# Kernel tuning notes

Hardware: AMD Instinct MI355X
Metric: run time of the kernel (lower is better)

Reference implementation:

```python
import jax, jax.numpy as jnp
import numpy as np

N_NODES = 100_000
N_EDGES = 3_200_000
IN_CH, HID, EMB = 8, 64, 32


def setup_inputs() -> dict:
    key = jax.random.key(0)
    ks = jax.random.split(key, 12)
    x = jax.random.normal(ks[0], (N_NODES, IN_CH), dtype=jnp.float32)
    edge_index = jax.random.randint(ks[1], (2, N_EDGES), 0, N_NODES, dtype=jnp.int64)
    s = 0.1
    return {
        "x": x,
        "edge_index": edge_index,
        # SAGEConv1: lin_l (neighbors, with bias), lin_r (root, no bias)
        "W1l": jax.random.normal(ks[2], (IN_CH, HID), jnp.float32) * s,
        "b1": jnp.zeros((HID,), jnp.float32),
        "W1r": jax.random.normal(ks[3], (IN_CH, HID), jnp.float32) * s,
        # SAGEConv2
        "W2l": jax.random.normal(ks[4], (HID, EMB), jnp.float32) * s,
        "b2": jnp.zeros((EMB,), jnp.float32),
        "W2r": jax.random.normal(ks[5], (HID, EMB), jnp.float32) * s,
        # head: Linear(32,16) ReLU Linear(16,1) Sigmoid
        "Wh1": jax.random.normal(ks[6], (EMB, 16), jnp.float32) * s,
        "bh1": jnp.zeros((16,), jnp.float32),
        "Wh2": jax.random.normal(ks[7], (16, 1), jnp.float32) * s,
        "bh2": jnp.zeros((1,), jnp.float32),
    }


def _sage_conv(x, src, dst, Wl, bl, Wr):
    # mean-aggregate source features at destination nodes
    msgs = x[src]                                            # [E, F]
    summed = jax.ops.segment_sum(msgs, dst, num_segments=N_NODES)
    cnt = jax.ops.segment_sum(jnp.ones((src.shape[0], 1), x.dtype), dst,
                              num_segments=N_NODES)
    aggr = summed / jnp.maximum(cnt, 1.0)                    # [N, F]
    return aggr @ Wl + bl + x @ Wr


def reference(x, edge_index, W1l, b1, W1r, W2l, b2, W2r, Wh1, bh1, Wh2, bh2):
    src, dst = edge_index[0], edge_index[1]
    h = jax.nn.relu(_sage_conv(x, src, dst, W1l, b1, W1r))   # [N, 64]
    z = jax.nn.relu(_sage_conv(h, src, dst, W2l, b2, W2r))   # [N, 32]
    logits = jax.nn.relu(z @ Wh1 + bh1) @ Wh2 + bh2          # [N, 1]
    return jax.nn.sigmoid(logits)[:, 0]                      # [N]
```

## Files before the change

kernel.cpp:

```cpp
#include <hip/hip_runtime.h>
#include <hip/hip_fp16.h>
#include <math.h>

#define IN_CH 8
#define HID   64
#define EMB   32
#define HBLK  256
#define BW    512
#define BSH   9
#define NBMAX 256
#define P8SCALE 128.0f
#define X8SCALE 16.0f

typedef _Float16 half2n __attribute__((ext_vector_type(2)));

static __device__ __forceinline__ __half2 u2h2(unsigned u) {
    union { unsigned u; __half2 h; } c; c.u = u; return c.h;
}
static __device__ __forceinline__ unsigned h22u(__half2 h) {
    union { unsigned u; __half2 h; } c; c.h = h; return c.u;
}
static __device__ __forceinline__ half2n u2n(unsigned u) {
    union { unsigned u; half2n h; } c; c.u = u; return c.h;
}
static __device__ __forceinline__ half2n mkh2(float a, float b) {
    half2n r; r.x = (_Float16)a; r.y = (_Float16)b; return r;
}
static __device__ __forceinline__ float fdot2w(half2n a, half2n b, float c) {
#if __has_builtin(__builtin_amdgcn_fdot2)
    return __builtin_amdgcn_fdot2(a, b, c, false);
#else
    return (float)a.x * (float)b.x + (float)a.y * (float)b.y + c;
#endif
}

__global__ __launch_bounds__(256) void histprep_kernel(
        const int* __restrict__ ei, int* __restrict__ gcnt, int* __restrict__ blkoff,
        int E, int NB, int per,
        const float* __restrict__ x, unsigned* __restrict__ x8,
        const float* __restrict__ W1l, const float* __restrict__ W1r,
        const float* __restrict__ W2l, const float* __restrict__ W2r,
        unsigned* __restrict__ w1p, unsigned* __restrict__ w2lp,
        unsigned* __restrict__ w2rp, int N) {
    __shared__ int lh[NBMAX];
    int b = blockIdx.x, t = threadIdx.x;
    if (b < HBLK) {
        for (int i = t; i < NB; i += 256) lh[i] = 0;
        __syncthreads();
        int e0 = b * per, e1 = min(e0 + per, E);
        if (e0 < e1) {
            if ((E & 3) == 0) {
                int nv = (e1 - e0) >> 2;
                for (int g = t; g < nv; g += 256) {
                    int4 d = *(const int4*)(ei + E + e0 + g * 4);
                    atomicAdd(&lh[d.x >> BSH], 1);
                    atomicAdd(&lh[d.y >> BSH], 1);
                    atomicAdd(&lh[d.z >> BSH], 1);
                    atomicAdd(&lh[d.w >> BSH], 1);
                }
                for (int e = e0 + nv * 4 + t; e < e1; e += 256)
                    atomicAdd(&lh[ei[E + e] >> BSH], 1);
            } else {
                for (int e = e0 + t; e < e1; e += 256)
                    atomicAdd(&lh[ei[E + e] >> BSH], 1);
            }
        }
        __syncthreads();
        for (int i = t; i < NB; i += 256)
            blkoff[b * NB + i] = atomicAdd(&gcnt[i], lh[i]);
        return;
    }
    int pb = b - HBLK;
    if (pb == 0) {
        for (int i = t; i < HID * IN_CH; i += 256) {
            int k = i >> 3, c = i & 7;
            w1p[i] = h22u(__floats2half2_rn(W1l[c * HID + k], W1r[c * HID + k]));
        }
        for (int i = t; i < (HID / 2) * EMB; i += 256) {
            int k2 = i >> 5, j = i & 31;
            w2lp[i] = h22u(__floats2half2_rn(W2l[(2 * k2) * EMB + j], W2l[(2 * k2 + 1) * EMB + j]));
            w2rp[i] = h22u(__floats2half2_rn(W2r[(2 * k2) * EMB + j], W2r[(2 * k2 + 1) * EMB + j]));
        }
    }
    int n = pb * 256 + t;
    if (n >= N) return;
    float4 a = ((const float4*)(x + (size_t)n * IN_CH))[0];
    float4 bb = ((const float4*)(x + (size_t)n * IN_CH))[1];
    float v[8] = {a.x, a.y, a.z, a.w, bb.x, bb.y, bb.z, bb.w};
    unsigned w0 = 0, w1 = 0;
    #pragma unroll
    for (int c = 0; c < 4; c++) {
        int q = min(127, max(-127, __float2int_rn(v[c] * X8SCALE))) + 128;
        w0 |= ((unsigned)q) << (8 * c);
    }
    #pragma unroll
    for (int c = 0; c < 4; c++) {
        int q = min(127, max(-127, __float2int_rn(v[4 + c] * X8SCALE))) + 128;
        w1 |= ((unsigned)q) << (8 * c);
    }
    ((uint2*)(x8 + (size_t)n * 2))[0] = make_uint2(w0, w1);
}

__global__ __launch_bounds__(256) void bscan_kernel(const int* __restrict__ gcnt,
                                                    int* __restrict__ sbase, int E, int NB) {
    __shared__ int bsum[256];
    int t = threadIdx.x;
    bsum[t] = (t < NB) ? gcnt[t] : 0;
    __syncthreads();
    for (int off = 1; off < 256; off <<= 1) {
        int v = (t >= off) ? bsum[t - off] : 0;
        __syncthreads();
        bsum[t] += v;
        __syncthreads();
    }
    if (t < NB) sbase[t] = bsum[t] - gcnt[t];
    if (t == 0) sbase[NB] = E;
}

__global__ __launch_bounds__(512) void scat_kernel(const int* __restrict__ ei,
                                                   const int* __restrict__ sbase,
                                                   const int* __restrict__ blkoff,
                                                   int* __restrict__ staged, int E, int NB,
                                                   int per) {
    __shared__ int lcur[NBMAX];
    int b = blockIdx.x, t = threadIdx.x;
    for (int i = t; i < NB; i += 512) lcur[i] = sbase[i] + blkoff[b * NB + i];
    __syncthreads();
    int e0 = b * per, e1 = min(e0 + per, E);
    if (e0 >= e1) return;
    if ((E & 3) == 0) {
        int nv = (e1 - e0) >> 2;
        for (int g = t; g < nv; g += 512) {
            int e = e0 + g * 4;
            int4 s4 = *(const int4*)(ei + e);
            int4 d4 = *(const int4*)(ei + E + e);
            int p0 = atomicAdd(&lcur[d4.x >> BSH], 1);
            staged[p0] = s4.x | ((d4.x & (BW - 1)) << 17);
            int p1 = atomicAdd(&lcur[d4.y >> BSH], 1);
            staged[p1] = s4.y | ((d4.y & (BW - 1)) << 17);
            int p2 = atomicAdd(&lcur[d4.z >> BSH], 1);
            staged[p2] = s4.z | ((d4.z & (BW - 1)) << 17);
            int p3 = atomicAdd(&lcur[d4.w >> BSH], 1);
            staged[p3] = s4.w | ((d4.w & (BW - 1)) << 17);
        }
        for (int e = e0 + nv * 4 + t; e < e1; e += 512) {
            int src = ei[e], dst = ei[E + e];
            int pos = atomicAdd(&lcur[dst >> BSH], 1);
            staged[pos] = src | ((dst & (BW - 1)) << 17);
        }
    } else {
        for (int e = e0 + t; e < e1; e += 512) {
            int src = ei[e], dst = ei[E + e];
            int pos = atomicAdd(&lcur[dst >> BSH], 1);
            staged[pos] = src | ((dst & (BW - 1)) << 17);
        }
    }
}

__global__ __launch_bounds__(1024) void bagg1_kernel(
        const int* __restrict__ staged, const int* __restrict__ sbase,
        const unsigned* __restrict__ x8,
        float* __restrict__ aggr, int* __restrict__ degb, int N, int NB) {
    __shared__ unsigned xs[BW * 5];
    __shared__ int ldeg[BW];
    int b = blockIdx.x, t = threadIdx.x;
    int base = b * BW;
    int s0 = sbase[b], s1 = sbase[b + 1];
    int len = s1 - s0;

    for (int i = t; i < BW * 5; i += 1024) xs[i] = 0u;
    if (t < BW) ldeg[t] = 0;
    __syncthreads();

    const unsigned M = 0x00FF00FFu;
    for (int i0 = t * 4; i0 < len; i0 += 4096) {
        int v0 = staged[s0 + i0];
        int v1 = (i0 + 1 < len) ? staged[s0 + i0 + 1] : -1;
        int v2 = (i0 + 2 < len) ? staged[s0 + i0 + 2] : -1;
        int v3 = (i0 + 3 < len) ? staged[s0 + i0 + 3] : -1;
        uint2 u0 = *(const uint2*)(x8 + (size_t)(v0 & 0x1FFFF) * 2);
        uint2 u1 = (v1 >= 0) ? *(const uint2*)(x8 + (size_t)(v1 & 0x1FFFF) * 2) : make_uint2(0, 0);
        uint2 u2 = (v2 >= 0) ? *(const uint2*)(x8 + (size_t)(v2 & 0x1FFFF) * 2) : make_uint2(0, 0);
        uint2 u3 = (v3 >= 0) ? *(const uint2*)(x8 + (size_t)(v3 & 0x1FFFF) * 2) : make_uint2(0, 0);
        {
            unsigned* xp = xs + (v0 >> 17) * 5;
            atomicAdd(xp + 0, u0.x & M); atomicAdd(xp + 1, (u0.x >> 8) & M);
            atomicAdd(xp + 2, u0.y & M); atomicAdd(xp + 3, (u0.y >> 8) & M);
            atomicAdd(&ldeg[v0 >> 17], 1);
        }
        if (v1 >= 0) {
            unsigned* xp = xs + (v1 >> 17) * 5;
            atomicAdd(xp + 0, u1.x & M); atomicAdd(xp + 1, (u1.x >> 8) & M);
            atomicAdd(xp + 2, u1.y & M); atomicAdd(xp + 3, (u1.y >> 8) & M);
            atomicAdd(&ldeg[v1 >> 17], 1);
        }
        if (v2 >= 0) {
            unsigned* xp = xs + (v2 >> 17) * 5;
            atomicAdd(xp + 0, u2.x & M); atomicAdd(xp + 1, (u2.x >> 8) & M);
            atomicAdd(xp + 2, u2.y & M); atomicAdd(xp + 3, (u2.y >> 8) & M);
            atomicAdd(&ldeg[v2 >> 17], 1);
        }
        if (v3 >= 0) {
            unsigned* xp = xs + (v3 >> 17) * 5;
            atomicAdd(xp + 0, u3.x & M); atomicAdd(xp + 1, (u3.x >> 8) & M);
            atomicAdd(xp + 2, u3.y & M); atomicAdd(xp + 3, (u3.y >> 8) & M);
            atomicAdd(&ldeg[v3 >> 17], 1);
        }
    }
    __syncthreads();

    if (t >= BW) return;
    int node = base + t;
    if (node >= N) return;
    int dg = ldeg[t];
    float bias = 128.0f * (float)dg;
    float inv = 1.0f / (X8SCALE * fmaxf((float)dg, 1.0f));
    unsigned Al0 = xs[t * 5 + 0], Ah0 = xs[t * 5 + 1];
    unsigned Al1 = xs[t * 5 + 2], Ah1 = xs[t * 5 + 3];
    float4 o0, o1;
    o0.x = ((float)(Al0 & 0xFFFF) - bias) * inv;
    o0.y = ((float)(Ah0 & 0xFFFF) - bias) * inv;
    o0.z = ((float)(Al0 >> 16) - bias) * inv;
    o0.w = ((float)(Ah0 >> 16) - bias) * inv;
    o1.x = ((float)(Al1 & 0xFFFF) - bias) * inv;
    o1.y = ((float)(Ah1 & 0xFFFF) - bias) * inv;
    o1.z = ((float)(Al1 >> 16) - bias) * inv;
    o1.w = ((float)(Ah1 >> 16) - bias) * inv;
    ((float4*)(aggr + (size_t)node * IN_CH))[0] = o0;
    ((float4*)(aggr + (size_t)node * IN_CH))[1] = o1;
    degb[node] = dg;
}

__global__ __launch_bounds__(256) void dense1b_kernel(
        const float* __restrict__ x, const float* __restrict__ aggr,
        const float* __restrict__ b1, const float* __restrict__ b2,
        const unsigned* __restrict__ w1p, const unsigned* __restrict__ w2lp,
        const unsigned* __restrict__ w2rp,
        unsigned* __restrict__ p8, unsigned* __restrict__ selfh, int N) {
    int t = threadIdx.x;
    int w = t >> 6;
    int lane = t & 63;
    int n = blockIdx.x * 64 + lane;
    if (n >= N) return;

    half2n uv[IN_CH];
    {
        float4 a0 = ((const float4*)(aggr + (size_t)n * IN_CH))[0];
        float4 a1 = ((const float4*)(aggr + (size_t)n * IN_CH))[1];
        float4 b0 = ((const float4*)(x + (size_t)n * IN_CH))[0];
        float4 b1v = ((const float4*)(x + (size_t)n * IN_CH))[1];
        uv[0] = mkh2(a0.x, b0.x); uv[1] = mkh2(a0.y, b0.y);
        uv[2] = mkh2(a0.z, b0.z); uv[3] = mkh2(a0.w, b0.w);
        uv[4] = mkh2(a1.x, b1v.x); uv[5] = mkh2(a1.y, b1v.y);
        uv[6] = mkh2(a1.z, b1v.z); uv[7] = mkh2(a1.w, b1v.w);
    }

    float pacc[8], sacc[8];
    const unsigned* w2lq = w2lp + w * 8;
    const unsigned* w2rq = w2rp + w * 8;
    #pragma unroll
    for (int j = 0; j < 8; j++) { pacc[j] = 0.0f; sacc[j] = b2[w * 8 + j]; }

    #pragma unroll 2
    for (int k2 = 0; k2 < HID / 2; k2++) {
        int k = 2 * k2;
        float h0 = b1[k], h1 = b1[k + 1];
        #pragma unroll
        for (int c = 0; c < IN_CH; c++) {
            h0 = fdot2w(uv[c], u2n(w1p[k * 8 + c]), h0);
            h1 = fdot2w(uv[c], u2n(w1p[(k + 1) * 8 + c]), h1);
        }
        h0 = fmaxf(h0, 0.0f);
        h1 = fmaxf(h1, 0.0f);
        half2n hh = mkh2(h0, h1);
        #pragma unroll
        for (int j = 0; j < 8; j++) {
            pacc[j] = fdot2w(hh, u2n(w2lq[k2 * EMB + j]), pacc[j]);
            sacc[j] = fdot2w(hh, u2n(w2rq[k2 * EMB + j]), sacc[j]);
        }
    }

    unsigned up[2];
    #pragma unroll
    for (int m = 0; m < 2; m++) {
        int q0 = min(127, max(-127, __float2int_rn(pacc[4 * m + 0] * P8SCALE)));
        int q1 = min(127, max(-127, __float2int_rn(pacc[4 * m + 1] * P8SCALE)));
        int q2 = min(127, max(-127, __float2int_rn(pacc[4 * m + 2] * P8SCALE)));
        int q3 = min(127, max(-127, __float2int_rn(pacc[4 * m + 3] * P8SCALE)));
        up[m] = ((unsigned)(q0 & 255) | ((unsigned)(q1 & 255) << 8)
              | ((unsigned)(q2 & 255) << 16) | ((unsigned)(q3 & 255) << 24)) ^ 0x80808080u;
    }
    ((uint2*)(p8 + (size_t)n * 8 + w * 2))[0] = make_uint2(up[0], up[1]);

    unsigned us[4];
    #pragma unroll
    for (int m = 0; m < 4; m++)
        us[m] = h22u(__floats2half2_rn(sacc[2 * m], sacc[2 * m + 1]));
    ((uint4*)(selfh + (size_t)n * 16 + w * 4))[0] = make_uint4(us[0], us[1], us[2], us[3]);
}

__global__ __launch_bounds__(1024) void bagg2_kernel(
        const int* __restrict__ staged, const int* __restrict__ sbase,
        const unsigned* __restrict__ p8, const unsigned* __restrict__ selfh,
        const int* __restrict__ degb,
        const float* __restrict__ Wh1, const float* __restrict__ bh1,
        const float* __restrict__ Wh2, const float* __restrict__ bh2,
        float* __restrict__ out, int N, int NB) {
    __shared__ unsigned zs[BW * 17];
    int b = blockIdx.x, t = threadIdx.x;
    int base = b * BW;
    int s0 = sbase[b], s1 = sbase[b + 1];
    int len = s1 - s0;

    for (int i = t; i < BW * 17; i += 1024) zs[i] = 0u;
    __syncthreads();

    const unsigned M = 0x00FF00FFu;
    for (int i0 = t * 4; i0 < len; i0 += 4096) {
        int v0 = staged[s0 + i0];
        int v1 = (i0 + 1 < len) ? staged[s0 + i0 + 1] : -1;
        int v2 = (i0 + 2 < len) ? staged[s0 + i0 + 2] : -1;
        int v3 = (i0 + 3 < len) ? staged[s0 + i0 + 3] : -1;
        const uint4* r0 = (const uint4*)(p8 + (size_t)(v0 & 0x1FFFF) * 8);
        uint4 a0 = r0[0], c0 = r0[1];
        uint4 a1, c1, a2, c2, a3, c3;
        if (v1 >= 0) { const uint4* r = (const uint4*)(p8 + (size_t)(v1 & 0x1FFFF) * 8); a1 = r[0]; c1 = r[1]; }
        if (v2 >= 0) { const uint4* r = (const uint4*)(p8 + (size_t)(v2 & 0x1FFFF) * 8); a2 = r[0]; c2 = r[1]; }
        if (v3 >= 0) { const uint4* r = (const uint4*)(p8 + (size_t)(v3 & 0x1FFFF) * 8); a3 = r[0]; c3 = r[1]; }
        {
            unsigned* zp = zs + (v0 >> 17) * 17;
            atomicAdd(zp + 0, a0.x & M);  atomicAdd(zp + 1, (a0.x >> 8) & M);
            atomicAdd(zp + 2, a0.y & M);  atomicAdd(zp + 3, (a0.y >> 8) & M);
            atomicAdd(zp + 4, a0.z & M);  atomicAdd(zp + 5, (a0.z >> 8) & M);
            atomicAdd(zp + 6, a0.w & M);  atomicAdd(zp + 7, (a0.w >> 8) & M);
            atomicAdd(zp + 8, c0.x & M);  atomicAdd(zp + 9, (c0.x >> 8) & M);
            atomicAdd(zp + 10, c0.y & M); atomicAdd(zp + 11, (c0.y >> 8) & M);
            atomicAdd(zp + 12, c0.z & M); atomicAdd(zp + 13, (c0.z >> 8) & M);
            atomicAdd(zp + 14, c0.w & M); atomicAdd(zp + 15, (c0.w >> 8) & M);
        }
        if (v1 >= 0) {
            unsigned* zp = zs + (v1 >> 17) * 17;
            atomicAdd(zp + 0, a1.x & M);  atomicAdd(zp + 1, (a1.x >> 8) & M);
            atomicAdd(zp + 2, a1.y & M);  atomicAdd(zp + 3, (a1.y >> 8) & M);
            atomicAdd(zp + 4, a1.z & M);  atomicAdd(zp + 5, (a1.z >> 8) & M);
            atomicAdd(zp + 6, a1.w & M);  atomicAdd(zp + 7, (a1.w >> 8) & M);
            atomicAdd(zp + 8, c1.x & M);  atomicAdd(zp + 9, (c1.x >> 8) & M);
            atomicAdd(zp + 10, c1.y & M); atomicAdd(zp + 11, (c1.y >> 8) & M);
            atomicAdd(zp + 12, c1.z & M); atomicAdd(zp + 13, (c1.z >> 8) & M);
            atomicAdd(zp + 14, c1.w & M); atomicAdd(zp + 15, (c1.w >> 8) & M);
        }
        if (v2 >= 0) {
            unsigned* zp = zs + (v2 >> 17) * 17;
            atomicAdd(zp + 0, a2.x & M);  atomicAdd(zp + 1, (a2.x >> 8) & M);
            atomicAdd(zp + 2, a2.y & M);  atomicAdd(zp + 3, (a2.y >> 8) & M);
            atomicAdd(zp + 4, a2.z & M);  atomicAdd(zp + 5, (a2.z >> 8) & M);
            atomicAdd(zp + 6, a2.w & M);  atomicAdd(zp + 7, (a2.w >> 8) & M);
            atomicAdd(zp + 8, c2.x & M);  atomicAdd(zp + 9, (c2.x >> 8) & M);
            atomicAdd(zp + 10, c2.y & M); atomicAdd(zp + 11, (c2.y >> 8) & M);
            atomicAdd(zp + 12, c2.z & M); atomicAdd(zp + 13, (c2.z >> 8) & M);
            atomicAdd(zp + 14, c2.w & M); atomicAdd(zp + 15, (c2.w >> 8) & M);
        }
        if (v3 >= 0) {
            unsigned* zp = zs + (v3 >> 17) * 17;
            atomicAdd(zp + 0, a3.x & M);  atomicAdd(zp + 1, (a3.x >> 8) & M);
            atomicAdd(zp + 2, a3.y & M);  atomicAdd(zp + 3, (a3.y >> 8) & M);
            atomicAdd(zp + 4, a3.z & M);  atomicAdd(zp + 5, (a3.z >> 8) & M);
            atomicAdd(zp + 6, a3.w & M);  atomicAdd(zp + 7, (a3.w >> 8) & M);
            atomicAdd(zp + 8, c3.x & M);  atomicAdd(zp + 9, (c3.x >> 8) & M);
            atomicAdd(zp + 10, c3.y & M); atomicAdd(zp + 11, (c3.y >> 8) & M);
            atomicAdd(zp + 12, c3.z & M); atomicAdd(zp + 13, (c3.z >> 8) & M);
            atomicAdd(zp + 14, c3.w & M); atomicAdd(zp + 15, (c3.w >> 8) & M);
        }
    }
    __syncthreads();

    if (t >= BW) return;
    int node = base + t;
    if (node >= N) return;
    int dg = degb[node];
    float bias = 128.0f * (float)dg;
    float sc = (1.0f / P8SCALE) / fmaxf((float)dg, 1.0f);

    float z[EMB];
    const uint2* sb = (const uint2*)(selfh + (size_t)node * 16);
    #pragma unroll
    for (int j = 0; j < 8; j++) {
        unsigned lo = zs[t * 17 + 2 * j];
        unsigned hi = zs[t * 17 + 2 * j + 1];
        uint2 sh = sb[j];
        float2 c0 = __half22float2(u2h2(sh.x));
        float2 c1 = __half22float2(u2h2(sh.y));
        z[4 * j + 0] = fmaxf(((float)(lo & 0xFFFF) - bias) * sc + c0.x, 0.0f);
        z[4 * j + 1] = fmaxf(((float)(hi & 0xFFFF) - bias) * sc + c0.y, 0.0f);
        z[4 * j + 2] = fmaxf(((float)(lo >> 16) - bias) * sc + c1.x, 0.0f);
        z[4 * j + 3] = fmaxf(((float)(hi >> 16) - bias) * sc + c1.y, 0.0f);
    }

    float logit = bh2[0];
    #pragma unroll
    for (int i = 0; i < 16; i++) {
        float acc = bh1[i];
        #pragma unroll
        for (int k = 0; k < EMB; k++) acc += z[k] * Wh1[k * 16 + i];
        logit += fmaxf(acc, 0.0f) * Wh2[i];
    }
    out[node] = 1.0f / (1.0f + expf(-logit));
}

extern "C" void kernel_launch(void* const* d_in, const int* in_sizes, int n_in,
                              void* d_out, int out_size, void* d_ws, size_t ws_size,
                              hipStream_t stream) {
    const float* x   = (const float*)d_in[0];
    const int*   ei  = (const int*)d_in[1];
    const float* W1l = (const float*)d_in[2];
    const float* b1  = (const float*)d_in[3];
    const float* W1r = (const float*)d_in[4];
    const float* W2l = (const float*)d_in[5];
    const float* b2  = (const float*)d_in[6];
    const float* W2r = (const float*)d_in[7];
    const float* Wh1 = (const float*)d_in[8];
    const float* bh1 = (const float*)d_in[9];
    const float* Wh2 = (const float*)d_in[10];
    const float* bh2 = (const float*)d_in[11];

    int N = in_sizes[0] / IN_CH;
    int E = in_sizes[1] / 2;
    int NB = (N + BW - 1) / BW;
    int M  = NB * HBLK;
    int per = (((E + HBLK - 1) / HBLK) + 3) & ~3;
    int PB = (N + 255) / 256;

    int N4 = (N + 3) & ~3;
    int NB4 = (NB + 3) & ~3;
    int* staged   = (int*)d_ws;
    int* blkoff   = staged + E;
    int* gcnt     = blkoff + M;
    int* sbase    = gcnt + NB4;
    int* degb     = sbase + NB4 + 4;
    unsigned* x8  = (unsigned*)(degb + N4);
    float* aggr   = (float*)(x8 + (size_t)(N + 2) * 2);
    unsigned* selfh = (unsigned*)(aggr + (size_t)N * IN_CH);
    unsigned* p8  = selfh + (size_t)N * 16;
    unsigned* w1p = p8 + (size_t)(N + 1) * 8 + 4;
    unsigned* w2lp = w1p + HID * IN_CH;
    unsigned* w2rp = w2lp + (HID / 2) * EMB;

    (void)hipMemsetAsync(gcnt, 0, sizeof(int) * NB4, stream);
    histprep_kernel<<<HBLK + PB, 256, 0, stream>>>(ei, gcnt, blkoff, E, NB, per,
                                                   x, x8, W1l, W1r, W2l, W2r,
                                                   w1p, w2lp, w2rp, N);
    bscan_kernel  <<<1, 256, 0, stream>>>(gcnt, sbase, E, NB);
    scat_kernel   <<<HBLK, 512, 0, stream>>>(ei, sbase, blkoff, staged, E, NB, per);
    bagg1_kernel  <<<NB, 1024, 0, stream>>>(staged, sbase, x8, aggr, degb, N, NB);
    dense1b_kernel<<<(N + 63) / 64, 256, 0, stream>>>(x, aggr, b1, b2,
                                                      w1p, w2lp, w2rp, p8, selfh, N);
    bagg2_kernel  <<<NB, 1024, 0, stream>>>(staged, sbase, p8, selfh, degb,
                                            Wh1, bh1, Wh2, bh2, (float*)d_out, N, NB);
}
```

Baseline: 119.0 us.

## Fuse dense layer-1 MLP into bagg1 epilogue, eliminating aggr buffer

Moves the dense1b computation (layer-1 linear+ReLU, then layer-2 projections quantized to p8/selfh) into the tail of bagg1, where each node's aggregated features are already in shared memory. All 1024 threads take part: each of the two 512-thread halves computes 16 of the 32 output channels for its node. This removes the float aggr intermediate round-trip through global memory and one kernel launch. In exchange, only NB (~196) blocks now run the dense math, so compute parallelism drops, each thread duplicates the full 64-wide hidden computation, and register pressure rises with 16+16 accumulators.

```diff
diff --git a/kernel.cpp b/kernel.cpp
--- a/kernel.cpp
+++ b/kernel.cpp
@@ -159,8 +159,12 @@
 
 __global__ __launch_bounds__(1024) void bagg1_kernel(
         const int* __restrict__ staged, const int* __restrict__ sbase,
-        const unsigned* __restrict__ x8,
-        float* __restrict__ aggr, int* __restrict__ degb, int N, int NB) {
+        const unsigned* __restrict__ x8, const float* __restrict__ x,
+        const float* __restrict__ b1, const float* __restrict__ b2,
+        const unsigned* __restrict__ w1p, const unsigned* __restrict__ w2lp,
+        const unsigned* __restrict__ w2rp,
+        unsigned* __restrict__ p8, unsigned* __restrict__ selfh,
+        int* __restrict__ degb, int N, int NB) {
     __shared__ unsigned xs[BW * 5];
     __shared__ int ldeg[BW];
     int b = blockIdx.x, t = threadIdx.x;
@@ -209,57 +213,42 @@
     }
     __syncthreads();
 
-    if (t >= BW) return;
-    int node = base + t;
+    int half = t >> 9;
+    int li = t & (BW - 1);
+    int node = base + li;
     if (node >= N) return;
-    int dg = ldeg[t];
+    int dg = ldeg[li];
+    if (half == 0) degb[node] = dg;
+
     float bias = 128.0f * (float)dg;
     float inv = 1.0f / (X8SCALE * fmaxf((float)dg, 1.0f));
-    unsigned Al0 = xs[t * 5 + 0], Ah0 = xs[t * 5 + 1];
-    unsigned Al1 = xs[t * 5 + 2], Ah1 = xs[t * 5 + 3];
-    float4 o0, o1;
-    o0.x = ((float)(Al0 & 0xFFFF) - bias) * inv;
-    o0.y = ((float)(Ah0 & 0xFFFF) - bias) * inv;
-    o0.z = ((float)(Al0 >> 16) - bias) * inv;
-    o0.w = ((float)(Ah0 >> 16) - bias) * inv;
-    o1.x = ((float)(Al1 & 0xFFFF) - bias) * inv;
-    o1.y = ((float)(Ah1 & 0xFFFF) - bias) * inv;
-    o1.z = ((float)(Al1 >> 16) - bias) * inv;
-    o1.w = ((float)(Ah1 >> 16) - bias) * inv;
-    ((float4*)(aggr + (size_t)node * IN_CH))[0] = o0;
-    ((float4*)(aggr + (size_t)node * IN_CH))[1] = o1;
-    degb[node] = dg;
-}
-
-__global__ __launch_bounds__(256) void dense1b_kernel(
-        const float* __restrict__ x, const float* __restrict__ aggr,
-        const float* __restrict__ b1, const float* __restrict__ b2,
-        const unsigned* __restrict__ w1p, const unsigned* __restrict__ w2lp,
-        const unsigned* __restrict__ w2rp,
-        unsigned* __restrict__ p8, unsigned* __restrict__ selfh, int N) {
-    int t = threadIdx.x;
-    int w = t >> 6;
-    int lane = t & 63;
-    int n = blockIdx.x * 64 + lane;
-    if (n >= N) return;
+    unsigned Al0 = xs[li * 5 + 0], Ah0 = xs[li * 5 + 1];
+    unsigned Al1 = xs[li * 5 + 2], Ah1 = xs[li * 5 + 3];
+    float av[IN_CH];
+    av[0] = ((float)(Al0 & 0xFFFF) - bias) * inv;
+    av[1] = ((float)(Ah0 & 0xFFFF) - bias) * inv;
+    av[2] = ((float)(Al0 >> 16) - bias) * inv;
+    av[3] = ((float)(Ah0 >> 16) - bias) * inv;
+    av[4] = ((float)(Al1 & 0xFFFF) - bias) * inv;
+    av[5] = ((float)(Ah1 & 0xFFFF) - bias) * inv;
+    av[6] = ((float)(Al1 >> 16) - bias) * inv;
+    av[7] = ((float)(Ah1 >> 16) - bias) * inv;
 
     half2n uv[IN_CH];
     {
-        float4 a0 = ((const float4*)(aggr + (size_t)n * IN_CH))[0];
-        float4 a1 = ((const float4*)(aggr + (size_t)n * IN_CH))[1];
-        float4 b0 = ((const float4*)(x + (size_t)n * IN_CH))[0];
-        float4 b1v = ((const float4*)(x + (size_t)n * IN_CH))[1];
-        uv[0] = mkh2(a0.x, b0.x); uv[1] = mkh2(a0.y, b0.y);
-        uv[2] = mkh2(a0.z, b0.z); uv[3] = mkh2(a0.w, b0.w);
-        uv[4] = mkh2(a1.x, b1v.x); uv[5] = mkh2(a1.y, b1v.y);
-        uv[6] = mkh2(a1.z, b1v.z); uv[7] = mkh2(a1.w, b1v.w);
-    }
-
-    float pacc[8], sacc[8];
-    const unsigned* w2lq = w2lp + w * 8;
-    const unsigned* w2rq = w2rp + w * 8;
-    #pragma unroll
-    for (int j = 0; j < 8; j++) { pacc[j] = 0.0f; sacc[j] = b2[w * 8 + j]; }
+        float4 b0 = ((const float4*)(x + (size_t)node * IN_CH))[0];
+        float4 b1v = ((const float4*)(x + (size_t)node * IN_CH))[1];
+        uv[0] = mkh2(av[0], b0.x); uv[1] = mkh2(av[1], b0.y);
+        uv[2] = mkh2(av[2], b0.z); uv[3] = mkh2(av[3], b0.w);
+        uv[4] = mkh2(av[4], b1v.x); uv[5] = mkh2(av[5], b1v.y);
+        uv[6] = mkh2(av[6], b1v.z); uv[7] = mkh2(av[7], b1v.w);
+    }
+
+    float pacc[16], sacc[16];
+    const unsigned* w2lh = w2lp + half * 16;
+    const unsigned* w2rh = w2rp + half * 16;
+    #pragma unroll
+    for (int j = 0; j < 16; j++) { pacc[j] = 0.0f; sacc[j] = b2[half * 16 + j]; }
 
     #pragma unroll 2
     for (int k2 = 0; k2 < HID / 2; k2++) {
@@ -274,15 +263,15 @@
         h1 = fmaxf(h1, 0.0f);
         half2n hh = mkh2(h0, h1);
         #pragma unroll
-        for (int j = 0; j < 8; j++) {
-            pacc[j] = fdot2w(hh, u2n(w2lq[k2 * EMB + j]), pacc[j]);
-            sacc[j] = fdot2w(hh, u2n(w2rq[k2 * EMB + j]), sacc[j]);
-        }
-    }
-
-    unsigned up[2];
-    #pragma unroll
-    for (int m = 0; m < 2; m++) {
+        for (int j = 0; j < 16; j++) {
+            pacc[j] = fdot2w(hh, u2n(w2lh[k2 * EMB + j]), pacc[j]);
+            sacc[j] = fdot2w(hh, u2n(w2rh[k2 * EMB + j]), sacc[j]);
+        }
+    }
+
+    unsigned up[4];
+    #pragma unroll
+    for (int m = 0; m < 4; m++) {
         int q0 = min(127, max(-127, __float2int_rn(pacc[4 * m + 0] * P8SCALE)));
         int q1 = min(127, max(-127, __float2int_rn(pacc[4 * m + 1] * P8SCALE)));
         int q2 = min(127, max(-127, __float2int_rn(pacc[4 * m + 2] * P8SCALE)));
@@ -290,13 +279,15 @@
         up[m] = ((unsigned)(q0 & 255) | ((unsigned)(q1 & 255) << 8)
               | ((unsigned)(q2 & 255) << 16) | ((unsigned)(q3 & 255) << 24)) ^ 0x80808080u;
     }
-    ((uint2*)(p8 + (size_t)n * 8 + w * 2))[0] = make_uint2(up[0], up[1]);
-
-    unsigned us[4];
-    #pragma unroll
-    for (int m = 0; m < 4; m++)
+    ((uint4*)(p8 + (size_t)node * 8 + half * 4))[0] = make_uint4(up[0], up[1], up[2], up[3]);
+
+    unsigned us[8];
+    #pragma unroll
+    for (int m = 0; m < 8; m++)
         us[m] = h22u(__floats2half2_rn(sacc[2 * m], sacc[2 * m + 1]));
-    ((uint4*)(selfh + (size_t)n * 16 + w * 4))[0] = make_uint4(us[0], us[1], us[2], us[3]);
+    uint4* sp = (uint4*)(selfh + (size_t)node * 16 + half * 8);
+    sp[0] = make_uint4(us[0], us[1], us[2], us[3]);
+    sp[1] = make_uint4(us[4], us[5], us[6], us[7]);
 }
 
 __global__ __launch_bounds__(1024) void bagg2_kernel(
@@ -438,8 +429,7 @@
     int* sbase    = gcnt + NB4;
     int* degb     = sbase + NB4 + 4;
     unsigned* x8  = (unsigned*)(degb + N4);
-    float* aggr   = (float*)(x8 + (size_t)(N + 2) * 2);
-    unsigned* selfh = (unsigned*)(aggr + (size_t)N * IN_CH);
+    unsigned* selfh = x8 + (size_t)(N + 2) * 2;
     unsigned* p8  = selfh + (size_t)N * 16;
     unsigned* w1p = p8 + (size_t)(N + 1) * 8 + 4;
     unsigned* w2lp = w1p + HID * IN_CH;
@@ -451,9 +441,8 @@
                                                    w1p, w2lp, w2rp, N);
     bscan_kernel  <<<1, 256, 0, stream>>>(gcnt, sbase, E, NB);
     scat_kernel   <<<HBLK, 512, 0, stream>>>(ei, sbase, blkoff, staged, E, NB, per);
-    bagg1_kernel  <<<NB, 1024, 0, stream>>>(staged, sbase, x8, aggr, degb, N, NB);
-    dense1b_kernel<<<(N + 63) / 64, 256, 0, stream>>>(x, aggr, b1, b2,
-                                                      w1p, w2lp, w2rp, p8, selfh, N);
+    bagg1_kernel  <<<NB, 1024, 0, stream>>>(staged, sbase, x8, x, b1, b2,
+                                            w1p, w2lp, w2rp, p8, selfh, degb, N, NB);
     bagg2_kernel  <<<NB, 1024, 0, stream>>>(staged, sbase, p8, selfh, degb,
                                             Wh1, bh1, Wh2, bh2, (float*)d_out, N, NB);
 }
```

Measured after the change: 130.3 us. +9.5%, slower.
